# Performance work log

Hardware: AMD Instinct MI355X
Metric: run time of the kernel (lower is better)

## Reference

```python
import jax, jax.numpy as jnp
import numpy as np

ALPHA = 0.2
NEG = -9e15


def _gru(x, Wih, Whh, bih, bhh):
    # x: [B, T, F]; PyTorch nn.GRU cell equations, scan over time.
    H = Whh.shape[1]
    xg = jnp.einsum('btf,gf->btg', x, Wih) + bih  # [B,T,3H]

    def step(h, gi):
        gh = h @ Whh.T + bhh
        ir, iz, inn = jnp.split(gi, 3, axis=-1)
        hr, hz, hn = jnp.split(gh, 3, axis=-1)
        r = jax.nn.sigmoid(ir + hr)
        z = jax.nn.sigmoid(iz + hz)
        n = jnp.tanh(inn + r * hn)
        h = (1.0 - z) * n + z * h
        return h, h

    h0 = jnp.zeros((x.shape[0], H), x.dtype)
    _, ys = jax.lax.scan(step, h0, jnp.swapaxes(xg, 0, 1))
    return jnp.swapaxes(ys, 0, 1)  # [B,T,H]


def _gru_attn(x, Wih, Whh, bih, bhh, aw, ab):
    out = _gru(x, Wih, Whh, bih, bhh)              # [B,T,H]
    w = jax.nn.softmax(out @ aw + ab, axis=1)       # [B,T,1]
    return jnp.sum(out * w, axis=1)                 # [B,H]


def _gat(h, mask, W, a):
    # GraphAttentionLayer with concat=True: elu(softmax(mask(leakyrelu(Wh1+Wh2^T))) @ Wh)
    Wh = h @ W                                      # [N,O]
    O = W.shape[1]
    e = jax.nn.leaky_relu((Wh @ a[:O]) + (Wh @ a[O:]).T, ALPHA)  # [N,N]
    att = jax.nn.softmax(jnp.where(mask, e, NEG), axis=1)
    return jax.nn.elu(att @ Wh)


def setup_inputs() -> dict:
    key = jax.random.key(0)
    ks = iter(jax.random.split(key, 40))
    B, S, Wk, D, F = 1, 2048, 32, 5, 16
    H, E, NS = 128, 128, 16

    def rn(shape, scale=0.1):
        return jax.random.normal(next(ks), shape, jnp.float32) * scale

    inp = {
        'stock_features': jax.random.normal(next(ks), (B, S, Wk, D, F), jnp.float32),
        'stock_to_sector': jax.random.randint(next(ks), (S,), 0, NS, jnp.int32),
        'inter_adj': jax.random.randint(next(ks), (NS, NS), 0, 2, jnp.int32),
        'gru1_Wih': rn((3 * H, F)), 'gru1_Whh': rn((3 * H, H)),
        'gru1_bih': rn((3 * H,)), 'gru1_bhh': rn((3 * H,)),
        'attn1_w': rn((H, 1)), 'attn1_b': rn((1,)),
        'gat_intra_W': rn((H, E)), 'gat_intra_a': rn((2 * E, 1)),
        'grug_Wih': rn((3 * E, E)), 'grug_Whh': rn((3 * E, E)),
        'grug_bih': rn((3 * E,)), 'grug_bhh': rn((3 * E,)),
        'attng_w': rn((E, 1)), 'attng_b': rn((1,)),
        'grua_Wih': rn((3 * E, H)), 'grua_Whh': rn((3 * E, E)),
        'grua_bih': rn((3 * E,)), 'grua_bhh': rn((3 * E,)),
        'attna_w': rn((E, 1)), 'attna_b': rn((1,)),
        'gat_inter_W': rn((E, E)), 'gat_inter_a': rn((2 * E, 1)),
        'fusion_w': rn((3 * E, E)), 'fusion_b': rn((E,)),
        'ret_w': rn((E, 1)), 'ret_b': rn((1,)),
        'mov_w': rn((E, 1)), 'mov_b': rn((1,)),
    }
    return inp


def reference(stock_features, stock_to_sector, inter_adj,
              gru1_Wih, gru1_Whh, gru1_bih, gru1_bhh, attn1_w, attn1_b,
              gat_intra_W, gat_intra_a,
              grug_Wih, grug_Whh, grug_bih, grug_bhh, attng_w, attng_b,
              grua_Wih, grua_Whh, grua_bih, grua_bhh, attna_w, attna_b,
              gat_inter_W, gat_inter_a,
              fusion_w, fusion_b, ret_w, ret_b, mov_w, mov_b):
    B, S, Wk, D, F = stock_features.shape
    H = gru1_Whh.shape[1]
    E = gat_intra_W.shape[1]
    NS = inter_adj.shape[0]

    # Short-term: GRU-attention over days, vectorized over (batch, stock, week).
    x = stock_features.reshape(B * S * Wk, D, F)
    short = _gru_attn(x, gru1_Wih, gru1_Whh, gru1_bih, gru1_bhh, attn1_w, attn1_b)
    short = short.reshape(B, S, Wk, H)

    # Intra-sector GAT on last-week embeddings; per-sector softmax == block mask.
    same_sector = stock_to_sector[:, None] == stock_to_sector[None, :]  # [S,S]
    last = short[:, :, -1, :]                                            # [B,S,H]
    intra = jax.vmap(lambda h: _gat(h, same_sector, gat_intra_W, gat_intra_a))(last)  # [B,S,E]

    # Long-term GRU-attentions.
    lg = _gru_attn(intra.reshape(B * S, 1, E), grug_Wih, grug_Whh, grug_bih, grug_bhh,
                   attng_w, attng_b).reshape(B, S, E)
    la = _gru_attn(short.reshape(B * S, Wk, H), grua_Wih, grua_Whh, grua_bih, grua_bhh,
                   attna_w, attna_b).reshape(B, S, E)

    # Sector embeddings = mean of stock long-term embeddings per sector.
    def sector_mean(g):
        sums = jax.ops.segment_sum(g, stock_to_sector, num_segments=NS)
        cnt = jax.ops.segment_sum(jnp.ones((g.shape[0], 1), g.dtype),
                                  stock_to_sector, num_segments=NS)
        return sums / jnp.maximum(cnt, 1.0)

    sec = jax.vmap(sector_mean)(lg)                                      # [B,NS,E]
    imask = inter_adj > 0
    sec_out = jax.vmap(lambda h: _gat(h, imask, gat_inter_W, gat_inter_a))(sec)
    sec_ps = sec_out[:, stock_to_sector, :]                               # [B,S,E]

    fused = jnp.concatenate([lg, la, sec_ps], axis=-1) @ fusion_w + fusion_b
    returns = (fused @ ret_w + ret_b)[..., 0]
    moves = jax.nn.sigmoid(fused @ mov_w + mov_b)[..., 0]
    return jnp.stack([returns, moves])  # [2,B,S]
```

## Files before the change

kernel.cpp:

```cpp
#include <hip/hip_runtime.h>
#include <math.h>

#define LRELU_A 0.2f
#define NEGBIG (-9.0e15f)

typedef _Float16 f16;
typedef _Float16 f16x8 __attribute__((ext_vector_type(8)));
typedef _Float16 f16x4 __attribute__((ext_vector_type(4)));
typedef float floatx4 __attribute__((ext_vector_type(4)));

__device__ __forceinline__ float rcpf(float x){ return __builtin_amdgcn_rcpf(x); }
__device__ __forceinline__ float sigm(float x){ return rcpf(1.0f+__expf(-x)); }
__device__ __forceinline__ float gru_fuse(float xr, float xz, float xn_pre, float ghn, float h){
    float Er = __expf(-xr);
    float r  = rcpf(1.0f + Er);
    float En = __expf(2.0f*(xn_pre + r*ghn));
    float Ez = __expf(-xz);
    float Dn = En + 1.0f;
    float num = fmaf(h, Dn, (En - 1.0f)*Ez);
    float den = Dn * (1.0f + Ez);
    return num * rcpf(den);
}
__device__ __forceinline__ f16x8 load_cvt8(const float* __restrict__ p){
    float4 a = *(const float4*)p; float4 b = *(const float4*)(p+4);
    f16x8 r; r[0]=(f16)a.x; r[1]=(f16)a.y; r[2]=(f16)a.z; r[3]=(f16)a.w;
    r[4]=(f16)b.x; r[5]=(f16)b.y; r[6]=(f16)b.z; r[7]=(f16)b.w;
    return r;
}
#define MFMA16(A,B,C) __builtin_amdgcn_mfma_f32_16x16x32_f16((A),(B),(C),0,0,0)

__global__ __launch_bounds__(256) void prep_kernel(
    const float* __restrict__ g1Wih, const float* __restrict__ g1Whh,
    const float* __restrict__ gaWih, const float* __restrict__ gaWhh,
    const float* __restrict__ giW,   const float* __restrict__ fw,
    const float* __restrict__ geW,
    const int* __restrict__ sec,
    f16* __restrict__ Wcat1, f16* __restrict__ WcatA,
    f16* __restrict__ WT, f16* __restrict__ fwT, f16* __restrict__ geWT,
    int* __restrict__ memflat, int* __restrict__ pos,
    int* __restrict__ cnt, int* __restrict__ base)
{
    __shared__ int cs[16], wsc[16];
    const int b = blockIdx.x, tid = threadIdx.x;
    if (b < 160){
        for (int idx = b*256+tid; idx < 512*160; idx += 160*256){
            int r = idx/160, k = idx - r*160;
            float v = 0.0f;
            if (r < 256){ if (k < 32){ if (k < 16) v = g1Wih[r*16+k]; } else v = g1Whh[r*128 + (k-32)]; }
            else if (r < 384){ if (k < 16) v = g1Wih[r*16+k]; }
            else { if (k >= 32) v = g1Whh[(r-128)*128 + (k-32)]; }
            Wcat1[idx] = (f16)v;
        }
    } else if (b < 416){
        for (int idx = (b-160)*256+tid; idx < 512*256; idx += 256*256){
            int r = idx >> 8, k = idx & 255;
            float v = 0.0f;
            if (r < 256){ v = (k < 128) ? gaWih[r*128+k] : gaWhh[r*128 + (k-128)]; }
            else if (r < 384){ if (k < 128) v = gaWih[r*128+k]; }
            else { if (k >= 128) v = gaWhh[(r-128)*128 + (k-128)]; }
            WcatA[idx] = (f16)v;
        }
    } else if (b < 480){
        int idx = (b-416)*256+tid;
        int r = idx >> 7, c = idx & 127;
        WT[c*128 + r] = (f16)giW[idx];
    } else if (b < 672){
        int idx = (b-480)*256+tid;
        int r = idx >> 7, c = idx & 127;
        fwT[c*384 + r] = (f16)fw[idx];
    } else if (b < 736){
        int idx = (b-672)*256+tid;
        int r = idx >> 7, c = idx & 127;
        geWT[c*128 + r] = (f16)geW[idx];
    } else {
        if (tid < 16) cs[tid] = 0;
        __syncthreads();
        for (int s = tid; s < 2048; s += 256) atomicAdd(&cs[sec[s]], 1);
        __syncthreads();
        if (tid == 0){
            int acc = 0;
            for (int g=0; g<16; g++){ cnt[g]=cs[g]; base[g]=acc; wsc[g]=acc; acc+=cs[g]; }
        }
        __syncthreads();
        for (int s = tid; s < 2048; s += 256){
            int g = sec[s];
            int p = atomicAdd(&wsc[g], 1);
            memflat[p] = s;
            pos[s] = p;
        }
    }
}

__global__ __launch_bounds__(512,2) void gru_short(
    const float* __restrict__ x, const f16* __restrict__ Wcat,
    const float* __restrict__ bih, const float* __restrict__ bhh,
    const float* __restrict__ aw, const float* __restrict__ ab,
    f16* __restrict__ out)
{
    __shared__ __align__(16) f16 xs[5][32][40];
    __shared__ __align__(16) f16 hs[2][32][136];
    __shared__ float scpart[2][8][32];
    const int tid = threadIdx.x, w = tid>>6, lane = tid&63;
    const int c = lane&15, quad = lane>>4;

    { f16x4 z4 = {0,0,0,0};
      f16x4* zx = (f16x4*)&xs[0][0][0];
      for (int i=tid; i<1600; i+=512) zx[i] = z4; }

    const int jrow = w*16 + c;
    f16x8 Ar[5], Az[5], Agi, Agh[4];
#pragma unroll
    for (int kb=0;kb<5;kb++){
        Ar[kb] = *(const f16x8*)&Wcat[(size_t)(jrow)*160 + kb*32 + quad*8];
        Az[kb] = *(const f16x8*)&Wcat[(size_t)(128+jrow)*160 + kb*32 + quad*8];
    }
    Agi = *(const f16x8*)&Wcat[(size_t)(256+jrow)*160 + quad*8];
#pragma unroll
    for (int i=0;i<4;i++)
        Agh[i] = *(const f16x8*)&Wcat[(size_t)(384+jrow)*160 + 32 + i*32 + quad*8];

    float brz_r[4], brz_z[4], b_in[4], b_hn[4], awr[4];
#pragma unroll
    for (int r=0;r<4;r++){
        int j = w*16 + quad*4 + r;
        brz_r[r] = bih[j] + bhh[j];
        brz_z[r] = bih[128+j] + bhh[128+j];
        b_in[r] = bih[256+j]; b_hn[r] = bhh[256+j];
        awr[r] = aw[j];
    }
    const float abv = ab[0];

    const int s0i = tid/20,        q0 = tid - 20*s0i;
    const int i1  = tid + 512;
    const int s1i = i1/20,         q1 = i1 - 20*s1i;
    const bool pf1 = (tid < 128);
    float4 xpf0, xpf1;
    {
        const size_t base0 = (size_t)(blockIdx.x*8)*32;
        xpf0 = *(const float4*)&x[(base0 + s0i)*80 + q0*4];
        if (pf1) xpf1 = *(const float4*)&x[(base0 + s1i)*80 + q1*4];
    }

#pragma unroll 1
    for (int tile=0; tile<8; ++tile){
        const int s0 = (blockIdx.x*8 + tile)*32;
        { f16x4 z4 = {0,0,0,0};
          f16x4* zh = (f16x4*)&hs[1][0][0];
          for (int i=tid; i<1088; i+=512) zh[i] = z4; }
        {
            int t = (q0*4)>>4, f = (q0*4)&15;
            f16x4 h4; h4[0]=(f16)xpf0.x; h4[1]=(f16)xpf0.y; h4[2]=(f16)xpf0.z; h4[3]=(f16)xpf0.w;
            *(f16x4*)&xs[t][s0i][f] = h4;
            if (pf1){
                int t1 = (q1*4)>>4, f1 = (q1*4)&15;
                f16x4 g4; g4[0]=(f16)xpf1.x; g4[1]=(f16)xpf1.y; g4[2]=(f16)xpf1.z; g4[3]=(f16)xpf1.w;
                *(f16x4*)&xs[t1][s1i][f1] = g4;
            }
        }
        if (tile < 7){
            const size_t basen = (size_t)(s0 + 32);
            xpf0 = *(const float4*)&x[(basen + s0i)*80 + q0*4];
            if (pf1) xpf1 = *(const float4*)&x[(basen + s1i)*80 + q1*4];
        }
        float hreg[2][4], aacc[2][4], l_[2] = {0.0f, 0.0f};
#pragma unroll
        for (int st=0; st<2; st++)
#pragma unroll
            for (int r=0;r<4;r++){ hreg[st][r]=0.0f; aacc[st][r]=0.0f; }
        __syncthreads();

#pragma unroll 1
        for (int t=0; t<5; ++t){
            const int rp = (t&1)^1, wp = t&1;
            f16x8 Bx[2], Bh[2][4];
#pragma unroll
            for (int st=0; st<2; st++){
                Bx[st] = *(const f16x8*)&xs[t][st*16+c][quad*8];
#pragma unroll
                for (int i=0;i<4;i++)
                    Bh[st][i] = *(const f16x8*)&hs[rp][st*16+c][i*32+quad*8];
            }
            if (t > 0){
#pragma unroll
                for (int st=0; st<2; st++){
                    float sc = abv;
#pragma unroll
                    for (int ww=0; ww<8; ww++) sc += scpart[rp][ww][st*16+c];
                    float e = __expf(sc);
                    l_[st] += e;
#pragma unroll
                    for (int r=0;r<4;r++) aacc[st][r] += e*hreg[st][r];
                }
            }
            float sp[2];
#pragma unroll
            for (int st=0; st<2; st++){
                floatx4 ar = {0,0,0,0}, az = {0,0,0,0}, agi = {0,0,0,0}, agh = {0,0,0,0};
                ar = MFMA16(Ar[0], Bx[st], ar);
                az = MFMA16(Az[0], Bx[st], az);
                agi = MFMA16(Agi, Bx[st], agi);
#pragma unroll
                for (int i=0;i<4;i++){
                    ar = MFMA16(Ar[1+i], Bh[st][i], ar);
                    az = MFMA16(Az[1+i], Bh[st][i], az);
                    agh = MFMA16(Agh[i], Bh[st][i], agh);
                }
                f16x4 h4;
                sp[st] = 0.0f;
#pragma unroll
                for (int r=0;r<4;r++){
                    float hn = gru_fuse(ar[r] + brz_r[r], az[r] + brz_z[r],
                                        agi[r] + b_in[r], agh[r] + b_hn[r], hreg[st][r]);
                    hreg[st][r] = hn; h4[r] = (f16)hn;
                    sp[st] += hn * awr[r];
                }
                *(f16x4*)&hs[wp][st*16 + c][w*16 + quad*4] = h4;
            }
#pragma unroll
            for (int st=0; st<2; st++){
                sp[st] += __shfl_xor(sp[st], 16);
                sp[st] += __shfl_xor(sp[st], 32);
            }
            if (lane < 16){ scpart[wp][w][lane] = sp[0]; scpart[wp][w][16+lane] = sp[1]; }
            __syncthreads();
        }
#pragma unroll
        for (int st=0; st<2; st++){
            float sc = abv;
#pragma unroll
            for (int ww=0; ww<8; ww++) sc += scpart[0][ww][st*16+c];
            float e = __expf(sc);
            l_[st] += e;
            float inv = rcpf(l_[st]);
            f16x4 h4;
#pragma unroll
            for (int r=0;r<4;r++) h4[r] = (f16)((aacc[st][r] + e*hreg[st][r])*inv);
            *(f16x4*)&hs[0][st*16 + c][w*16 + quad*4] = h4;
        }
        __syncthreads();
        { int s = tid>>4, p = tid&15;
          *(f16x8*)&out[(size_t)(s0+s)*128 + p*8] = *(const f16x8*)&hs[0][s][p*8]; }
    }
}

__global__ __launch_bounds__(512,2) void gru_la_gatprep(
    const f16* __restrict__ xseq, const f16* __restrict__ Wcat,
    const float* __restrict__ bih, const float* __restrict__ bhh,
    const float* __restrict__ aw, const float* __restrict__ ab,
    f16* __restrict__ out,
    const f16* __restrict__ WT, const float* __restrict__ gia,
    const int* __restrict__ memflat,
    f16* __restrict__ Whs, float* __restrict__ ers, float* __restrict__ el)
{
    __shared__ __align__(16) f16 xs[2][16][136];
    __shared__ __align__(16) f16 hs[2][16][136];
    __shared__ float scpart[2][8][16];
    __shared__ __align__(16) float tbuf[32][132];
    __shared__ int rows[32];
    const int tid = threadIdx.x, w = tid>>6, lane = tid&63;
    const int c = lane&15, quad = lane>>4;

    if (blockIdx.x >= 256){
        const int p0 = (blockIdx.x-256)*32;
        if (tid < 32) rows[tid] = memflat[p0 + tid];
        __syncthreads();
        f16x8 A[2][4];
#pragma unroll
        for (int mt=0;mt<2;mt++)
#pragma unroll
            for (int kb=0;kb<4;kb++)
                A[mt][kb] = *(const f16x8*)&xseq[((size_t)rows[mt*16+c]*32 + 31)*128 + kb*32 + quad*8];
        {
            int jb = w;
            f16x8 B[4];
#pragma unroll
            for (int kb=0;kb<4;kb++)
                B[kb] = *(const f16x8*)&WT[(size_t)(jb*16+c)*128 + kb*32 + quad*8];
            floatx4 acc[2] = {{0,0,0,0},{0,0,0,0}};
#pragma unroll
            for (int kb=0;kb<4;kb++){
                acc[0] = MFMA16(A[0][kb], B[kb], acc[0]);
                acc[1] = MFMA16(A[1][kb], B[kb], acc[1]);
            }
#pragma unroll
            for (int mt=0;mt<2;mt++)
#pragma unroll
                for (int r=0;r<4;r++)
                    tbuf[mt*16 + quad*4 + r][jb*16 + c] = acc[mt][r];
        }
        __syncthreads();
        for (int i=tid; i<1024; i+=512){
            int s = i>>5, p = i&31;
            float4 v = *(const float4*)&tbuf[s][p*4];
            f16x4 h4; h4[0]=(f16)v.x; h4[1]=(f16)v.y; h4[2]=(f16)v.z; h4[3]=(f16)v.w;
            *(f16x4*)&Whs[(size_t)(p0+s)*128 + p*4] = h4;
        }
        for (int k=0; k<4; k++){
            int row = w*4 + k;
            float w0 = tbuf[row][lane], w1 = tbuf[row][64+lane];
            float v1 = w0*gia[lane]     + w1*gia[64+lane];
            float v2 = w0*gia[128+lane] + w1*gia[192+lane];
#pragma unroll
            for (int off=32; off; off>>=1){ v1 += __shfl_down(v1,off); v2 += __shfl_down(v2,off); }
            if (lane==0){ el[rows[row]] = v1; ers[p0+row] = v2; }
        }
        return;
    }
    const int s0 = blockIdx.x*8;
    { f16x4 z4 = {0,0,0,0};
      f16x4* za = (f16x4*)&xs[0][0][0];
      for (int i=tid; i<1088; i+=512) za[i] = z4;
      f16x4* zh = (f16x4*)&hs[0][0][0];
      for (int i=tid; i<1088; i+=512) zh[i] = z4; }
    __syncthreads();
    if (tid < 128){
        int s = tid>>4, p = tid&15;
        *(f16x8*)&xs[0][s][p*8] = *(const f16x8*)&xseq[((size_t)(s0+s)*32 + 0)*128 + p*8];
    }
    const int jrow = w*16 + c;
    f16x8 Ar[8], Az[8], Agi[4], Agh[4];
#pragma unroll
    for (int kb=0;kb<8;kb++){
        Ar[kb] = *(const f16x8*)&Wcat[(size_t)(jrow)*256 + kb*32 + quad*8];
        Az[kb] = *(const f16x8*)&Wcat[(size_t)(128+jrow)*256 + kb*32 + quad*8];
    }
#pragma unroll
    for (int i=0;i<4;i++){
        Agi[i] = *(const f16x8*)&Wcat[(size_t)(256+jrow)*256 + i*32 + quad*8];
        Agh[i] = *(const f16x8*)&Wcat[(size_t)(384+jrow)*256 + 128 + i*32 + quad*8];
    }
    float brz_r[4], brz_z[4], b_in[4], b_hn[4], awr[4];
#pragma unroll
    for (int r=0;r<4;r++){
        int j = w*16 + quad*4 + r;
        brz_r[r] = bih[j] + bhh[j];
        brz_z[r] = bih[128+j] + bhh[128+j];
        b_in[r] = bih[256+j]; b_hn[r] = bhh[256+j];
        awr[r] = aw[j];
    }
    const float abv = ab[0];
    float hreg[4] = {0,0,0,0}, aacc[4] = {0,0,0,0}, l_ = 0.0f;
    __syncthreads();

#pragma unroll 1
    for (int t=0; t<32; ++t){
        const int rp = (t&1)^1, wp = t&1, xp = t&1;
        f16x8 Bx[4], Bh[4];
#pragma unroll
        for (int i=0;i<4;i++){
            Bx[i] = *(const f16x8*)&xs[xp][c][i*32+quad*8];
            Bh[i] = *(const f16x8*)&hs[rp][c][i*32+quad*8];
        }
        f16x8 xstage;
        const bool do_stage = (t < 31) && (tid < 128);
        if (do_stage){
            int s = tid>>4, p = tid&15;
            xstage = *(const f16x8*)&xseq[((size_t)(s0+s)*32 + t+1)*128 + p*8];
        }
        if (t > 0){
            float sc = abv;
#pragma unroll
            for (int ww=0; ww<8; ww++) sc += scpart[rp][ww][c];
            float e = __expf(sc);
            l_ += e;
#pragma unroll
            for (int r=0;r<4;r++) aacc[r] += e*hreg[r];
        }
        floatx4 ar = {0,0,0,0}, az = {0,0,0,0}, agi = {0,0,0,0}, agh = {0,0,0,0};
#pragma unroll
        for (int i=0;i<4;i++){
            ar = MFMA16(Ar[i], Bx[i], ar);
            az = MFMA16(Az[i], Bx[i], az);
            agi = MFMA16(Agi[i], Bx[i], agi);
        }
#pragma unroll
        for (int i=0;i<4;i++){
            ar = MFMA16(Ar[4+i], Bh[i], ar);
            az = MFMA16(Az[4+i], Bh[i], az);
            agh = MFMA16(Agh[i], Bh[i], agh);
        }
        f16x4 h4;
        float sp = 0.0f;
#pragma unroll
        for (int r=0;r<4;r++){
            float hn = gru_fuse(ar[r] + brz_r[r], az[r] + brz_z[r],
                                agi[r] + b_in[r], agh[r] + b_hn[r], hreg[r]);
            hreg[r] = hn; h4[r] = (f16)hn;
            sp += hn * awr[r];
        }
        *(f16x4*)&hs[wp][c][w*16 + quad*4] = h4;
        if (do_stage){
            int s = tid>>4, p = tid&15;
            *(f16x8*)&xs[xp^1][s][p*8] = xstage;
        }
        sp += __shfl_xor(sp, 16);
        sp += __shfl_xor(sp, 32);
        if (lane < 16) scpart[wp][w][lane] = sp;
        __syncthreads();
    }
    {
        float sc = abv;
#pragma unroll
        for (int ww=0; ww<8; ww++) sc += scpart[1][ww][c];
        float e = __expf(sc);
        l_ += e;
        float inv = rcpf(l_);
        f16x4 h4;
#pragma unroll
        for (int r=0;r<4;r++) h4[r] = (f16)((aacc[r] + e*hreg[r])*inv);
        *(f16x4*)&hs[1][c][w*16 + quad*4] = h4;
    }
    __syncthreads();
    if (tid < 128){
        int s = tid>>4, p = tid&15;
        *(f16x8*)&out[(size_t)(s0+s)*128 + p*8] = *(const f16x8*)&hs[1][s][p*8];
    }
}

__global__ __launch_bounds__(256) void gat_intra_mem_kernel(
    const f16* __restrict__ Whs, const float* __restrict__ ers,
    const float* __restrict__ el, const int* __restrict__ sec,
    const int* __restrict__ cnt, const int* __restrict__ base,
    f16* __restrict__ outp, int S)
{
    int wave = threadIdx.x>>6, lane = threadIdx.x&63;
    int i = blockIdx.x*4 + wave;
    if (i>=S) return;
    int g = sec[i];
    int n = cnt[g], b = base[g];
    float eli = el[i];
    float m = -INFINITY;
    for (int jj=lane; jj<n; jj+=64){
        float v = eli + ers[b+jj]; v = v>0.f? v : LRELU_A*v;
        m = fmaxf(m, v);
    }
#pragma unroll
    for (int off=32; off; off>>=1) m = fmaxf(m, __shfl_xor(m, off));
    float l = 0.f, c0=0.f, c1=0.f;
#pragma unroll 4
    for (int jj=0; jj<n; jj++){
        float v = eli + ers[b+jj]; v = v>0.f? v : LRELU_A*v;
        float p = __expf(v-m);
        l += p;
        c0 += p*(float)Whs[(size_t)(b+jj)*128 + lane];
        c1 += p*(float)Whs[(size_t)(b+jj)*128 + 64 + lane];
    }
    float il = rcpf(l);
    c0 *= il; c1 *= il;
    outp[(size_t)i*128+lane]    = (f16)(c0>0.f? c0 : expm1f(c0));
    outp[(size_t)i*128+64+lane] = (f16)(c1>0.f? c1 : expm1f(c1));
}

__global__ __launch_bounds__(256) void lg_mfma(
    const f16* __restrict__ intra16, const float* __restrict__ Wih,
    const float* __restrict__ bih, const float* __restrict__ bhh,
    const int* __restrict__ pos,
    f16* __restrict__ lgout, f16* __restrict__ lgs)
{
    __shared__ __align__(16) f16 tbuf[32][136];
    const int tid = threadIdx.x, w = tid>>6, lane = tid&63;
    const int c = lane&15, quad = lane>>4;
    const int s0 = blockIdx.x*32;
    f16x8 A[2][4];
#pragma unroll
    for (int mt=0;mt<2;mt++)
#pragma unroll
        for (int kb=0;kb<4;kb++)
            A[mt][kb] = *(const f16x8*)&intra16[(size_t)(s0+mt*16+c)*128 + kb*32 + quad*8];
#pragma unroll
    for (int i=0;i<2;i++){
        int jb = w*2 + i;
        int j = jb*16 + c;
        f16x8 Br[4], Bz[4], Bn[4];
#pragma unroll
        for (int kb=0;kb<4;kb++){
            Br[kb] = load_cvt8(&Wih[(size_t)(j)*128 + kb*32 + quad*8]);
            Bz[kb] = load_cvt8(&Wih[(size_t)(128+j)*128 + kb*32 + quad*8]);
            Bn[kb] = load_cvt8(&Wih[(size_t)(256+j)*128 + kb*32 + quad*8]);
        }
        float b_r = bih[j] + bhh[j];
        float b_z = bih[128+j] + bhh[128+j];
        float b_i = bih[256+j], b_h = bhh[256+j];
        floatx4 ar[2] = {{0,0,0,0},{0,0,0,0}};
        floatx4 az[2] = {{0,0,0,0},{0,0,0,0}};
        floatx4 an[2] = {{0,0,0,0},{0,0,0,0}};
#pragma unroll
        for (int kb=0;kb<4;kb++)
#pragma unroll
            for (int mt=0;mt<2;mt++){
                ar[mt] = MFMA16(A[mt][kb], Br[kb], ar[mt]);
                az[mt] = MFMA16(A[mt][kb], Bz[kb], az[mt]);
                an[mt] = MFMA16(A[mt][kb], Bn[kb], an[mt]);
            }
#pragma unroll
        for (int mt=0;mt<2;mt++)
#pragma unroll
            for (int r=0;r<4;r++){
                float Er = __expf(-(ar[mt][r] + b_r));
                float rg = rcpf(1.0f + Er);
                float En = __expf(2.0f*(an[mt][r] + b_i + rg*b_h));
                float Ez = __expf(-(az[mt][r] + b_z));
                float v = (En - 1.0f)*Ez * rcpf((En + 1.0f)*(1.0f + Ez));
                tbuf[mt*16 + quad*4 + r][j] = (f16)v;
            }
    }
    __syncthreads();
    for (int i=tid; i<512; i+=256){
        int s = i>>4, p = i&15;
        f16x8 v = *(const f16x8*)&tbuf[s][p*8];
        *(f16x8*)&lgout[(size_t)(s0+s)*128 + p*8] = v;
        *(f16x8*)&lgs[(size_t)pos[s0+s]*128 + p*8] = v;
    }
}

__global__ __launch_bounds__(1024) void gat_inter_fused(
    const f16* __restrict__ lgs, const int* __restrict__ cnt,
    const int* __restrict__ base, const int* __restrict__ adj,
    const f16* __restrict__ geWT, const float* __restrict__ a,
    float* __restrict__ outp)
{
    __shared__ __align__(16) float hs[16][132];
    __shared__ __align__(16) float Whs[16][132];
    __shared__ float el[16], er[16];
    __shared__ float att[16][16];
    const int tid = threadIdx.x, w = tid>>6, lane = tid&63;
    const int c = lane&15, quad = lane>>4;

    {
        int n = cnt[w], b = base[w];
        const int rowoff = lane>>4;
        const int colb = (lane&15)*8;
        float acc[8] = {0,0,0,0,0,0,0,0};
        for (int r = rowoff; r < n; r += 4){
            f16x8 v = *(const f16x8*)&lgs[(size_t)(b+r)*128 + colb];
#pragma unroll
            for (int k=0;k<8;k++) acc[k] += (float)v[k];
        }
#pragma unroll
        for (int k=0;k<8;k++){
            acc[k] += __shfl_xor(acc[k], 16);
            acc[k] += __shfl_xor(acc[k], 32);
        }
        if (lane < 16){
            float inv = rcpf(fmaxf((float)n, 1.0f));
#pragma unroll
            for (int k=0;k<8;k++) hs[w][colb+k] = acc[k]*inv;
        }
    }
    __syncthreads();
    if (w < 8){
        f16x8 A[4], B[4];
#pragma unroll
        for (int kb=0;kb<4;kb++){
            A[kb] = load_cvt8(&hs[c][kb*32 + quad*8]);
            B[kb] = *(const f16x8*)&geWT[(size_t)(w*16+c)*128 + kb*32 + quad*8];
        }
        floatx4 acc = {0,0,0,0};
#pragma unroll
        for (int kb=0;kb<4;kb++) acc = MFMA16(A[kb], B[kb], acc);
#pragma unroll
        for (int r=0;r<4;r++) Whs[quad*4 + r][w*16 + c] = acc[r];
    }
    __syncthreads();
    {
        int half = lane>>5, l = lane&31;
        const float* av = a + half*128;
        float acc2 = 0.f;
#pragma unroll
        for (int k=0;k<4;k++) acc2 += Whs[w][l+32*k]*av[l+32*k];
#pragma unroll
        for (int off=1; off<32; off<<=1) acc2 += __shfl_xor(acc2, off);
        if (l==0){ if (half) er[w]=acc2; else el[w]=acc2; }
    }
    __syncthreads();
    if (tid<16){
        int i=tid; float m=NEGBIG; float e[16];
        for(int j=0;j<16;j++){
            float v = el[i]+er[j]; v = v>0.f? v : LRELU_A*v;
            e[j] = (adj[i*16+j]>0)? v : NEGBIG;
            m = fmaxf(m,e[j]);
        }
        float l=0.f;
        for(int j=0;j<16;j++){ float p=__expf(e[j]-m); att[i][j]=p; l+=p; }
        float il = rcpf(l);
        for(int j=0;j<16;j++) att[i][j] *= il;
    }
    __syncthreads();
#pragma unroll
    for (int i=0;i<2;i++){
        int idx=i*1024+tid; int o=idx&127, s=idx>>7;
        float acc=0.f;
#pragma unroll
        for(int j=0;j<16;j++) acc += att[s][j]*Whs[j][o];
        outp[s*128+o] = acc>0.f? acc : expm1f(acc);
    }
}

__global__ __launch_bounds__(256) void fused_mfma(
    const f16* __restrict__ lg16, const f16* __restrict__ la16,
    const float* __restrict__ seco, const int* __restrict__ sec,
    const f16* __restrict__ fwT,
    const float* __restrict__ fb, const float* __restrict__ rw,
    const float* __restrict__ rb, const float* __restrict__ mw,
    const float* __restrict__ mb, float* __restrict__ outp)
{
    __shared__ float rpart[4][32], mpart[4][32];
    const int tid = threadIdx.x, w = tid>>6, lane = tid&63;
    const int c = lane&15, quad = lane>>4;
    const int s0 = blockIdx.x*32;
    f16x8 A[2][12];
#pragma unroll
    for (int mt=0;mt<2;mt++){
        int row = s0 + mt*16 + c;
        int g = sec[row];
#pragma unroll
        for (int kb=0;kb<4;kb++){
            A[mt][kb]   = *(const f16x8*)&lg16[(size_t)row*128 + kb*32 + quad*8];
            A[mt][4+kb] = *(const f16x8*)&la16[(size_t)row*128 + kb*32 + quad*8];
            A[mt][8+kb] = load_cvt8(&seco[(size_t)g*128 + kb*32 + quad*8]);
        }
    }
    float rsum[2][4] = {{0,0,0,0},{0,0,0,0}};
    float msum[2][4] = {{0,0,0,0},{0,0,0,0}};
#pragma unroll
    for (int i=0;i<2;i++){
        int jb = w*2 + i;
        int col = jb*16 + c;
        f16x8 B[12];
#pragma unroll
        for (int kb=0;kb<12;kb++)
            B[kb] = *(const f16x8*)&fwT[(size_t)col*384 + kb*32 + quad*8];
        floatx4 acc[2] = {{0,0,0,0},{0,0,0,0}};
#pragma unroll
        for (int kb=0;kb<12;kb++){
            acc[0] = MFMA16(A[0][kb], B[kb], acc[0]);
            acc[1] = MFMA16(A[1][kb], B[kb], acc[1]);
        }
        float fbv = fb[col], rwv = rw[col], mwv = mw[col];
#pragma unroll
        for (int mt=0;mt<2;mt++)
#pragma unroll
            for (int r=0;r<4;r++){
                float fu = acc[mt][r] + fbv;
                rsum[mt][r] += fu*rwv;
                msum[mt][r] += fu*mwv;
            }
    }
#pragma unroll
    for (int mt=0;mt<2;mt++)
#pragma unroll
        for (int r=0;r<4;r++){
#pragma unroll
            for (int off=1; off<16; off<<=1){
                rsum[mt][r] += __shfl_xor(rsum[mt][r], off);
                msum[mt][r] += __shfl_xor(msum[mt][r], off);
            }
            if (c==0){
                rpart[w][mt*16 + quad*4 + r] = rsum[mt][r];
                mpart[w][mt*16 + quad*4 + r] = msum[mt][r];
            }
        }
    __syncthreads();
    if (tid < 32){
        int s = tid;
        float rs = rb[0], ms = mb[0];
#pragma unroll
        for (int ww=0; ww<4; ww++){ rs += rpart[ww][s]; ms += mpart[ww][s]; }
        outp[s0+s] = rs;
        outp[2048 + s0 + s] = sigm(ms);
    }
}

extern "C" void kernel_launch(void* const* d_in, const int* in_sizes, int n_in,
                              void* d_out, int out_size, void* d_ws, size_t ws_size,
                              hipStream_t stream) {
    const float* sf    = (const float*)d_in[0];
    const int*   sec   = (const int*)  d_in[1];
    const int*   adj   = (const int*)  d_in[2];
    const float* g1Wih = (const float*)d_in[3];
    const float* g1Whh = (const float*)d_in[4];
    const float* g1bih = (const float*)d_in[5];
    const float* g1bhh = (const float*)d_in[6];
    const float* a1w   = (const float*)d_in[7];
    const float* a1b   = (const float*)d_in[8];
    const float* giW   = (const float*)d_in[9];
    const float* gia   = (const float*)d_in[10];
    const float* ggWih = (const float*)d_in[11];
    const float* ggbih = (const float*)d_in[13];
    const float* ggbhh = (const float*)d_in[14];
    const float* gaWih = (const float*)d_in[17];
    const float* gaWhh = (const float*)d_in[18];
    const float* gabih = (const float*)d_in[19];
    const float* gabhh = (const float*)d_in[20];
    const float* aaw   = (const float*)d_in[21];
    const float* aab   = (const float*)d_in[22];
    const float* geW   = (const float*)d_in[23];
    const float* gea   = (const float*)d_in[24];
    const float* fw    = (const float*)d_in[25];
    const float* fb    = (const float*)d_in[26];
    const float* rw    = (const float*)d_in[27];
    const float* rb    = (const float*)d_in[28];
    const float* mw    = (const float*)d_in[29];
    const float* mb    = (const float*)d_in[30];

    char* p = (char*)d_ws;
    f16*   shrt16 = (f16*)p;   p += (size_t)65536*128*2;
    f16*   intra16= (f16*)p;   p += (size_t)262144*2;
    f16*   lg16   = (f16*)p;   p += (size_t)262144*2;
    f16*   la16   = (f16*)p;   p += (size_t)262144*2;
    f16*   Whs    = (f16*)p;   p += (size_t)262144*2;
    f16*   lgs    = (f16*)p;   p += (size_t)262144*2;
    f16*   Wcat1  = (f16*)p;   p += (size_t)512*160*2;
    f16*   WcatA  = (f16*)p;   p += (size_t)512*256*2;
    f16*   WT     = (f16*)p;   p += (size_t)16384*2;
    f16*   geWT   = (f16*)p;   p += (size_t)16384*2;
    f16*   fwT    = (f16*)p;   p += (size_t)49152*2;
    float* el     = (float*)p; p += 2048*4;
    float* ers    = (float*)p; p += 2048*4;
    float* seco   = (float*)p; p += 2048*4;
    int*   memflat= (int*)p;   p += 2048*4;
    int*   pos    = (int*)p;   p += 2048*4;
    int*   cnt    = (int*)p;   p += 16*4;
    int*   basep  = (int*)p;   p += 16*4;

    prep_kernel<<<737,256,0,stream>>>(g1Wih, g1Whh, gaWih, gaWhh, giW, fw, geW, sec,
                                      Wcat1, WcatA, WT, fwT, geWT, memflat, pos, cnt, basep);
    gru_short<<<256,512,0,stream>>>(sf, Wcat1, g1bih, g1bhh, a1w, a1b, shrt16);
    gru_la_gatprep<<<320,512,0,stream>>>(shrt16, WcatA, gabih, gabhh, aaw, aab, la16,
                                         WT, gia, memflat, Whs, ers, el);
    gat_intra_mem_kernel<<<512,256,0,stream>>>(Whs, ers, el, sec, cnt, basep, intra16, 2048);
    lg_mfma<<<64,256,0,stream>>>(intra16, ggWih, ggbih, ggbhh, pos, lg16, lgs);
    gat_inter_fused<<<1,1024,0,stream>>>(lgs, cnt, basep, adj, geWT, gea, seco);
    fused_mfma<<<64,256,0,stream>>>(lg16, la16, seco, sec, fwT, fb, rw, rb, mw, mb, (float*)d_out);
}
```

Measured before the change: 299.0 us.

## Reorder kernels so GRU-attention overlaps the single-block inter-sector GAT

The GAT-prep blocks are split out of the la-GRU kernel into their own kernel, which now runs before the intra GAT. The la-GRU recurrence runs after lg_mfma and carries one extra block that computes the inter-sector GAT. The serial single-block gat_inter kernel now runs alongside the 256 GRU blocks instead of as its own launch with the GPU mostly idle. The cost is that GAT-prep no longer overlaps with the GRU. The extra block also does its sector work with 8 warps instead of 16.

```diff
diff --git a/kernel.cpp b/kernel.cpp
--- a/kernel.cpp
+++ b/kernel.cpp
@@ -243,66 +243,150 @@
     }
 }
 
-__global__ __launch_bounds__(512,2) void gru_la_gatprep(
+__global__ __launch_bounds__(512) void gat_prep_k(
+    const f16* __restrict__ shrt16, const f16* __restrict__ WT,
+    const float* __restrict__ gia, const int* __restrict__ memflat,
+    f16* __restrict__ Whs, float* __restrict__ ers, float* __restrict__ el)
+{
+    __shared__ __align__(16) float tbuf[32][132];
+    __shared__ int rows[32];
+    const int tid = threadIdx.x, w = tid>>6, lane = tid&63;
+    const int c = lane&15, quad = lane>>4;
+    const int p0 = blockIdx.x*32;
+    if (tid < 32) rows[tid] = memflat[p0 + tid];
+    __syncthreads();
+    f16x8 A[2][4];
+#pragma unroll
+    for (int mt=0;mt<2;mt++)
+#pragma unroll
+        for (int kb=0;kb<4;kb++)
+            A[mt][kb] = *(const f16x8*)&shrt16[((size_t)rows[mt*16+c]*32 + 31)*128 + kb*32 + quad*8];
+    {
+        int jb = w;
+        f16x8 B[4];
+#pragma unroll
+        for (int kb=0;kb<4;kb++)
+            B[kb] = *(const f16x8*)&WT[(size_t)(jb*16+c)*128 + kb*32 + quad*8];
+        floatx4 acc[2] = {{0,0,0,0},{0,0,0,0}};
+#pragma unroll
+        for (int kb=0;kb<4;kb++){
+            acc[0] = MFMA16(A[0][kb], B[kb], acc[0]);
+            acc[1] = MFMA16(A[1][kb], B[kb], acc[1]);
+        }
+#pragma unroll
+        for (int mt=0;mt<2;mt++)
+#pragma unroll
+            for (int r=0;r<4;r++)
+                tbuf[mt*16 + quad*4 + r][jb*16 + c] = acc[mt][r];
+    }
+    __syncthreads();
+    for (int i=tid; i<1024; i+=512){
+        int s = i>>5, p = i&31;
+        float4 v = *(const float4*)&tbuf[s][p*4];
+        f16x4 h4; h4[0]=(f16)v.x; h4[1]=(f16)v.y; h4[2]=(f16)v.z; h4[3]=(f16)v.w;
+        *(f16x4*)&Whs[(size_t)(p0+s)*128 + p*4] = h4;
+    }
+    for (int k=0; k<4; k++){
+        int row = w*4 + k;
+        float w0 = tbuf[row][lane], w1 = tbuf[row][64+lane];
+        float v1 = w0*gia[lane]     + w1*gia[64+lane];
+        float v2 = w0*gia[128+lane] + w1*gia[192+lane];
+#pragma unroll
+        for (int off=32; off; off>>=1){ v1 += __shfl_down(v1,off); v2 += __shfl_down(v2,off); }
+        if (lane==0){ el[rows[row]] = v1; ers[p0+row] = v2; }
+    }
+}
+
+__global__ __launch_bounds__(512,2) void gru_la_tail(
     const f16* __restrict__ xseq, const f16* __restrict__ Wcat,
     const float* __restrict__ bih, const float* __restrict__ bhh,
     const float* __restrict__ aw, const float* __restrict__ ab,
     f16* __restrict__ out,
-    const f16* __restrict__ WT, const float* __restrict__ gia,
-    const int* __restrict__ memflat,
-    f16* __restrict__ Whs, float* __restrict__ ers, float* __restrict__ el)
+    const f16* __restrict__ lgs, const int* __restrict__ cnt,
+    const int* __restrict__ base, const int* __restrict__ adj,
+    const f16* __restrict__ geWT, const float* __restrict__ a,
+    float* __restrict__ seco)
 {
     __shared__ __align__(16) f16 xs[2][16][136];
     __shared__ __align__(16) f16 hs[2][16][136];
     __shared__ float scpart[2][8][16];
-    __shared__ __align__(16) float tbuf[32][132];
-    __shared__ int rows[32];
+    __shared__ __align__(16) float ths[16][132];
+    __shared__ __align__(16) float tWhs[16][132];
+    __shared__ float tel[16], ter[16];
+    __shared__ float tatt[16][16];
     const int tid = threadIdx.x, w = tid>>6, lane = tid&63;
     const int c = lane&15, quad = lane>>4;
 
-    if (blockIdx.x >= 256){
-        const int p0 = (blockIdx.x-256)*32;
-        if (tid < 32) rows[tid] = memflat[p0 + tid];
-        __syncthreads();
-        f16x8 A[2][4];
-#pragma unroll
-        for (int mt=0;mt<2;mt++)
-#pragma unroll
-            for (int kb=0;kb<4;kb++)
-                A[mt][kb] = *(const f16x8*)&xseq[((size_t)rows[mt*16+c]*32 + 31)*128 + kb*32 + quad*8];
+    if (blockIdx.x == 256){
+#pragma unroll 1
+        for (int g = w; g < 16; g += 8){
+            int n = cnt[g], b = base[g];
+            const int rowoff = lane>>4;
+            const int colb = (lane&15)*8;
+            float acc[8] = {0,0,0,0,0,0,0,0};
+            for (int r = rowoff; r < n; r += 4){
+                f16x8 v = *(const f16x8*)&lgs[(size_t)(b+r)*128 + colb];
+#pragma unroll
+                for (int k=0;k<8;k++) acc[k] += (float)v[k];
+            }
+#pragma unroll
+            for (int k=0;k<8;k++){
+                acc[k] += __shfl_xor(acc[k], 16);
+                acc[k] += __shfl_xor(acc[k], 32);
+            }
+            if (lane < 16){
+                float inv = rcpf(fmaxf((float)n, 1.0f));
+#pragma unroll
+                for (int k=0;k<8;k++) ths[g][colb+k] = acc[k]*inv;
+            }
+        }
+        __syncthreads();
         {
-            int jb = w;
-            f16x8 B[4];
-#pragma unroll
-            for (int kb=0;kb<4;kb++)
-                B[kb] = *(const f16x8*)&WT[(size_t)(jb*16+c)*128 + kb*32 + quad*8];
-            floatx4 acc[2] = {{0,0,0,0},{0,0,0,0}};
+            f16x8 A[4], B[4];
 #pragma unroll
             for (int kb=0;kb<4;kb++){
-                acc[0] = MFMA16(A[0][kb], B[kb], acc[0]);
-                acc[1] = MFMA16(A[1][kb], B[kb], acc[1]);
-            }
-#pragma unroll
-            for (int mt=0;mt<2;mt++)
-#pragma unroll
-                for (int r=0;r<4;r++)
-                    tbuf[mt*16 + quad*4 + r][jb*16 + c] = acc[mt][r];
-        }
-        __syncthreads();
-        for (int i=tid; i<1024; i+=512){
-            int s = i>>5, p = i&31;
-            float4 v = *(const float4*)&tbuf[s][p*4];
-            f16x4 h4; h4[0]=(f16)v.x; h4[1]=(f16)v.y; h4[2]=(f16)v.z; h4[3]=(f16)v.w;
-            *(f16x4*)&Whs[(size_t)(p0+s)*128 + p*4] = h4;
-        }
-        for (int k=0; k<4; k++){
-            int row = w*4 + k;
-            float w0 = tbuf[row][lane], w1 = tbuf[row][64+lane];
-            float v1 = w0*gia[lane]     + w1*gia[64+lane];
-            float v2 = w0*gia[128+lane] + w1*gia[192+lane];
-#pragma unroll
-            for (int off=32; off; off>>=1){ v1 += __shfl_down(v1,off); v2 += __shfl_down(v2,off); }
-            if (lane==0){ el[rows[row]] = v1; ers[p0+row] = v2; }
+                A[kb] = load_cvt8(&ths[c][kb*32 + quad*8]);
+                B[kb] = *(const f16x8*)&geWT[(size_t)(w*16+c)*128 + kb*32 + quad*8];
+            }
+            floatx4 acc = {0,0,0,0};
+#pragma unroll
+            for (int kb=0;kb<4;kb++) acc = MFMA16(A[kb], B[kb], acc);
+#pragma unroll
+            for (int r=0;r<4;r++) tWhs[quad*4 + r][w*16 + c] = acc[r];
+        }
+        __syncthreads();
+#pragma unroll 1
+        for (int g = w; g < 16; g += 8){
+            int half = lane>>5, l = lane&31;
+            const float* av = a + half*128;
+            float acc2 = 0.f;
+#pragma unroll
+            for (int k=0;k<4;k++) acc2 += tWhs[g][l+32*k]*av[l+32*k];
+#pragma unroll
+            for (int off=1; off<32; off<<=1) acc2 += __shfl_xor(acc2, off);
+            if (l==0){ if (half) ter[g]=acc2; else tel[g]=acc2; }
+        }
+        __syncthreads();
+        if (tid<16){
+            int i=tid; float m=NEGBIG; float e[16];
+            for(int j=0;j<16;j++){
+                float v = tel[i]+ter[j]; v = v>0.f? v : LRELU_A*v;
+                e[j] = (adj[i*16+j]>0)? v : NEGBIG;
+                m = fmaxf(m,e[j]);
+            }
+            float l=0.f;
+            for(int j=0;j<16;j++){ float p=__expf(e[j]-m); tatt[i][j]=p; l+=p; }
+            float il = rcpf(l);
+            for(int j=0;j<16;j++) tatt[i][j] *= il;
+        }
+        __syncthreads();
+#pragma unroll
+        for (int i=0;i<4;i++){
+            int idx=i*512+tid; int o=idx&127, s=idx>>7;
+            float acc=0.f;
+#pragma unroll
+            for(int j=0;j<16;j++) acc += tatt[s][j]*tWhs[j][o];
+            seco[s*128+o] = acc>0.f? acc : expm1f(acc);
         }
         return;
     }
@@ -510,89 +594,6 @@
         f16x8 v = *(const f16x8*)&tbuf[s][p*8];
         *(f16x8*)&lgout[(size_t)(s0+s)*128 + p*8] = v;
         *(f16x8*)&lgs[(size_t)pos[s0+s]*128 + p*8] = v;
-    }
-}
-
-__global__ __launch_bounds__(1024) void gat_inter_fused(
-    const f16* __restrict__ lgs, const int* __restrict__ cnt,
-    const int* __restrict__ base, const int* __restrict__ adj,
-    const f16* __restrict__ geWT, const float* __restrict__ a,
-    float* __restrict__ outp)
-{
-    __shared__ __align__(16) float hs[16][132];
-    __shared__ __align__(16) float Whs[16][132];
-    __shared__ float el[16], er[16];
-    __shared__ float att[16][16];
-    const int tid = threadIdx.x, w = tid>>6, lane = tid&63;
-    const int c = lane&15, quad = lane>>4;
-
-    {
-        int n = cnt[w], b = base[w];
-        const int rowoff = lane>>4;
-        const int colb = (lane&15)*8;
-        float acc[8] = {0,0,0,0,0,0,0,0};
-        for (int r = rowoff; r < n; r += 4){
-            f16x8 v = *(const f16x8*)&lgs[(size_t)(b+r)*128 + colb];
-#pragma unroll
-            for (int k=0;k<8;k++) acc[k] += (float)v[k];
-        }
-#pragma unroll
-        for (int k=0;k<8;k++){
-            acc[k] += __shfl_xor(acc[k], 16);
-            acc[k] += __shfl_xor(acc[k], 32);
-        }
-        if (lane < 16){
-            float inv = rcpf(fmaxf((float)n, 1.0f));
-#pragma unroll
-            for (int k=0;k<8;k++) hs[w][colb+k] = acc[k]*inv;
-        }
-    }
-    __syncthreads();
-    if (w < 8){
-        f16x8 A[4], B[4];
-#pragma unroll
-        for (int kb=0;kb<4;kb++){
-            A[kb] = load_cvt8(&hs[c][kb*32 + quad*8]);
-            B[kb] = *(const f16x8*)&geWT[(size_t)(w*16+c)*128 + kb*32 + quad*8];
-        }
-        floatx4 acc = {0,0,0,0};
-#pragma unroll
-        for (int kb=0;kb<4;kb++) acc = MFMA16(A[kb], B[kb], acc);
-#pragma unroll
-        for (int r=0;r<4;r++) Whs[quad*4 + r][w*16 + c] = acc[r];
-    }
-    __syncthreads();
-    {
-        int half = lane>>5, l = lane&31;
-        const float* av = a + half*128;
-        float acc2 = 0.f;
-#pragma unroll
-        for (int k=0;k<4;k++) acc2 += Whs[w][l+32*k]*av[l+32*k];
-#pragma unroll
-        for (int off=1; off<32; off<<=1) acc2 += __shfl_xor(acc2, off);
-        if (l==0){ if (half) er[w]=acc2; else el[w]=acc2; }
-    }
-    __syncthreads();
-    if (tid<16){
-        int i=tid; float m=NEGBIG; float e[16];
-        for(int j=0;j<16;j++){
-            float v = el[i]+er[j]; v = v>0.f? v : LRELU_A*v;
-            e[j] = (adj[i*16+j]>0)? v : NEGBIG;
-            m = fmaxf(m,e[j]);
-        }
-        float l=0.f;
-        for(int j=0;j<16;j++){ float p=__expf(e[j]-m); att[i][j]=p; l+=p; }
-        float il = rcpf(l);
-        for(int j=0;j<16;j++) att[i][j] *= il;
-    }
-    __syncthreads();
-#pragma unroll
-    for (int i=0;i<2;i++){
-        int idx=i*1024+tid; int o=idx&127, s=idx>>7;
-        float acc=0.f;
-#pragma unroll
-        for(int j=0;j<16;j++) acc += att[s][j]*Whs[j][o];
-        outp[s*128+o] = acc>0.f? acc : expm1f(acc);
     }
 }
 
@@ -726,10 +727,10 @@
     prep_kernel<<<737,256,0,stream>>>(g1Wih, g1Whh, gaWih, gaWhh, giW, fw, geW, sec,
                                       Wcat1, WcatA, WT, fwT, geWT, memflat, pos, cnt, basep);
     gru_short<<<256,512,0,stream>>>(sf, Wcat1, g1bih, g1bhh, a1w, a1b, shrt16);
-    gru_la_gatprep<<<320,512,0,stream>>>(shrt16, WcatA, gabih, gabhh, aaw, aab, la16,
-                                         WT, gia, memflat, Whs, ers, el);
+    gat_prep_k<<<64,512,0,stream>>>(shrt16, WT, gia, memflat, Whs, ers, el);
     gat_intra_mem_kernel<<<512,256,0,stream>>>(Whs, ers, el, sec, cnt, basep, intra16, 2048);
     lg_mfma<<<64,256,0,stream>>>(intra16, ggWih, ggbih, ggbhh, pos, lg16, lgs);
-    gat_inter_fused<<<1,1024,0,stream>>>(lgs, cnt, basep, adj, geWT, gea, seco);
+    gru_la_tail<<<257,512,0,stream>>>(shrt16, WcatA, gabih, gabhh, aaw, aab, la16,
+                                      lgs, cnt, basep, adj, geWT, gea, seco);
     fused_mfma<<<64,256,0,stream>>>(lg16, la16, seco, sec, fwT, fb, rw, rb, mw, mb, (float*)d_out);
 }
```

New measurement: 305.0 us. 2.0% more time.
